# Kernel tuning notes

Measured on AMD Instinct MI355X. Metric: run time of the kernel, lower is better.

Reference implementation:

```python
import jax, jax.numpy as jnp
import numpy as np

N, F, H, D = 50000, 128, 8, 16   # nodes, node features, heads, per-head dim (F == H*D -> Identity residual)
E, G = 800000, 512               # edges, graphs
HD = H * D


def _xavier(key, shape):
    fan = sum(shape[-2:]) if len(shape) >= 2 else shape[0] + 1
    lim = (6.0 / (shape[-2] + shape[-1])) ** 0.5 if len(shape) >= 2 else (6.0 / fan) ** 0.5
    return jax.random.uniform(key, shape, jnp.float32, -lim, lim)


def setup_inputs() -> dict:
    key = jax.random.key(0)
    ks = jax.random.split(key, 10)
    x = jax.random.normal(ks[0], (N, F), jnp.float32)
    edge_index = jax.random.randint(ks[1], (2, E), 0, N, dtype=jnp.int64)
    batch = jnp.sort(jax.random.randint(ks[2], (N,), 0, G, dtype=jnp.int64))
    W_src = _xavier(ks[3], (HD, F))
    W_dst = _xavier(ks[4], (HD, F))
    double_attn = _xavier(ks[5], (1, H, D))  # xavier over last two dims
    bias = jnp.zeros((HD,), jnp.float32)
    prelu_alpha = jnp.float32(0.25)          # nn.PReLU() default single weight
    w_weighting = _xavier(ks[6], (1, HD))
    b_weighting = jnp.zeros((1,), jnp.float32)
    w_score = _xavier(ks[7], (HD, HD))
    b_score = jnp.zeros((HD,), jnp.float32)
    return {
        "x": x, "edge_index": edge_index, "batch": batch,
        "W_src": W_src, "W_dst": W_dst, "double_attn": double_attn,
        "bias": bias, "prelu_alpha": prelu_alpha,
        "w_weighting": w_weighting, "b_weighting": b_weighting,
        "w_score": w_score, "b_score": b_score,
    }


def reference(x, edge_index, batch, W_src, W_dst, double_attn, bias, prelu_alpha,
              w_weighting, b_weighting, w_score, b_score):
    src, dst = edge_index[0], edge_index[1]
    # dropout is identity in eval mode
    src_p = (x @ W_src.T).reshape(N, H, D)    # [N,H,D]
    dst_p = (x @ W_dst.T).reshape(N, H, D)
    # edge-wise attention logits: gather + LeakyReLU(0.2) + dot with attention vector
    e = src_p[src] + dst_p[dst]               # [E,H,D]
    e = jnp.where(e > 0, e, 0.2 * e)
    logits = jnp.einsum('ehd,ohd->eh', e, double_attn)  # [E,H] (double_attn has leading 1)
    # segment softmax over destination nodes (global max shift, as in original)
    exp = jnp.exp(logits - logits.max())
    denom = jax.ops.segment_sum(exp, dst, num_segments=N)  # [N,H]
    alpha = exp / (denom[dst] + 1e-16)        # [E,H]
    # weighted aggregation of source projections
    msg = src_p[src] * alpha[:, :, None]      # [E,H,D]
    out = jax.ops.segment_sum(msg, dst, num_segments=N)    # [N,H,D]
    out = out + x.reshape(N, H, D)            # residual (Identity since F == H*D)
    out = out.reshape(N, HD) + bias           # concat heads + bias
    out = jnp.where(out > 0, out, prelu_alpha * out)       # PReLU activation
    # ReadoutPhase: gated sum pooling + max pooling per graph, concatenated
    weighted = jax.nn.sigmoid(out @ w_weighting.T + b_weighting)  # [N,1]
    score = out @ w_score.T + b_score                              # [N,HD]
    g_sum = jax.ops.segment_sum(weighted * score, batch, num_segments=G)  # [G,HD]
    g_max = jax.ops.segment_max(out, batch, num_segments=G)              # [G,HD]
    readout = jnp.concatenate([g_sum, g_max], axis=1)                     # [G,2*HD]
    return out, readout
```

## Files before the change

kernel.cpp:

```cpp
#include <hip/hip_runtime.h>

#define NODES 50000
#define FEAT 128
#define EDGES 800000
#define GRAPHS 512
#define NB 196
#define CHUNK 4096
#define ABLK 196
#define BCAP 8192
#define PROJ_BLOCKS 782

typedef unsigned int u32;
typedef unsigned short u16;
typedef __attribute__((ext_vector_type(8))) short short8;
typedef __attribute__((ext_vector_type(4))) float v4f;
typedef __attribute__((ext_vector_type(4))) u32 u32x4;
typedef __attribute__((ext_vector_type(2))) float f2;

static __device__ __forceinline__ float bflo(u32 u){ return __uint_as_float(u << 16); }
static __device__ __forceinline__ float bfhi(u32 u){ return __uint_as_float(u & 0xffff0000u); }
static __device__ __forceinline__ u16 f2bf(float f){
  u32 u = __float_as_uint(f);
  u32 r = u + 0x7fffu + ((u >> 16) & 1u);
  return (u16)(r >> 16);
}
static __device__ __forceinline__ u32 packbf(float a, float b){
  return (u32)f2bf(a) | ((u32)f2bf(b) << 16);
}
static __device__ __forceinline__ f2 unpk(u32 u){ f2 r; r.x = bflo(u); r.y = bfhi(u); return r; }
static __device__ __forceinline__ f2 vmax2(f2 a, f2 b){ f2 r; r.x = fmaxf(a.x,b.x); r.y = fmaxf(a.y,b.y); return r; }

#define LROW 68
__global__ __launch_bounds__(256) void proj_hist_kernel(
    const float* __restrict__ x, const float* __restrict__ Wsrc,
    const float* __restrict__ Wdst, u16* __restrict__ srcp, u16* __restrict__ dstp,
    const int* __restrict__ ei, int* __restrict__ bcount)
{
  __shared__ u32 x_lds[64 * LROW];
  __shared__ int cnt[NB];
  const int t = threadIdx.x;

  if (blockIdx.x >= PROJ_BLOCKS){
    const int b = blockIdx.x - PROJ_BLOCKS;
    for (int k = t; k < NB; k += 256) cnt[k] = 0;
    __syncthreads();
    const int e0 = b * CHUNK;
    const int e1 = (e0 + CHUNK < EDGES) ? e0 + CHUNK : EDGES;
    for (int e = e0 + t; e < e1; e += 256)
      atomicAdd(&cnt[ei[EDGES + e] >> 8], 1);
    __syncthreads();
    for (int k = t; k < NB; k += 256) bcount[k * ABLK + b] = cnt[k];
    return;
  }

  const int node0 = blockIdx.x * 64;
  const int rows_valid = NODES - node0 < 64 ? NODES - node0 : 64;
  const float4* xp = (const float4*)(x + (size_t)node0 * 128);
  for (int idx = t; idx < rows_valid * 32; idx += 256){
    const float4 v = xp[idx];
    const int row = idx >> 5, cq = idx & 31;
    x_lds[row * LROW + cq * 2]     = packbf(v.x, v.y);
    x_lds[row * LROW + cq * 2 + 1] = packbf(v.z, v.w);
  }

  const int wave = t >> 6, lane = t & 63;
  const int r16 = lane & 15;
  const int quad = lane >> 4;
  const int ko = quad * 4;
  const int n0 = wave * 32;

  short8 bs[2][4], bd[2][4];
  #pragma unroll
  for (int nt = 0; nt < 2; ++nt){
    const int col = n0 + nt * 16 + r16;
    #pragma unroll
    for (int k = 0; k < 4; ++k){
      const float4* wp = (const float4*)(Wsrc + col * 128 + quad * 8 + k * 32);
      float4 w0 = wp[0], w1 = wp[1];
      u32x4 pk; pk.x = packbf(w0.x,w0.y); pk.y = packbf(w0.z,w0.w);
      pk.z = packbf(w1.x,w1.y); pk.w = packbf(w1.z,w1.w);
      bs[nt][k] = __builtin_bit_cast(short8, pk);
      const float4* vp = (const float4*)(Wdst + col * 128 + quad * 8 + k * 32);
      float4 v0 = vp[0], v1 = vp[1];
      u32x4 qk; qk.x = packbf(v0.x,v0.y); qk.y = packbf(v0.z,v0.w);
      qk.z = packbf(v1.x,v1.y); qk.w = packbf(v1.z,v1.w);
      bd[nt][k] = __builtin_bit_cast(short8, qk);
    }
  }
  __syncthreads();

  #pragma unroll
  for (int mt = 0; mt < 4; ++mt){
    const int node_base = node0 + mt * 16;
    if (node_base >= NODES) break;
    short8 afr[4];
    #pragma unroll
    for (int k = 0; k < 4; ++k)
      afr[k] = *(const short8*)&x_lds[(mt * 16 + r16) * LROW + ko + k * 16];
    v4f s0 = {0.f,0.f,0.f,0.f}, s1 = s0, d0 = s0, d1 = s0;
    #pragma unroll
    for (int k = 0; k < 4; ++k){
      s0 = __builtin_amdgcn_mfma_f32_16x16x32_bf16(afr[k], bs[0][k], s0, 0, 0, 0);
      s1 = __builtin_amdgcn_mfma_f32_16x16x32_bf16(afr[k], bs[1][k], s1, 0, 0, 0);
      d0 = __builtin_amdgcn_mfma_f32_16x16x32_bf16(afr[k], bd[0][k], d0, 0, 0, 0);
      d1 = __builtin_amdgcn_mfma_f32_16x16x32_bf16(afr[k], bd[1][k], d1, 0, 0, 0);
    }
    u16* so = srcp + (size_t)(node_base + quad * 4) * 128 + n0 + r16;
    u16* do_ = dstp + (size_t)(node_base + quad * 4) * 128 + n0 + r16;
    #pragma unroll
    for (int r = 0; r < 4; ++r){
      so[r * 128]      = f2bf(s0[r]);
      so[r * 128 + 16] = f2bf(s1[r]);
      do_[r * 128]      = f2bf(d0[r]);
      do_[r * 128 + 16] = f2bf(d1[r]);
    }
  }
}

__global__ __launch_bounds__(256) void bucket_scatter_kernel(
    const int* __restrict__ ei, const int* __restrict__ bcount,
    int* __restrict__ bstart_g, u32* __restrict__ ebuf)
{
  __shared__ int tot[256];
  __shared__ int bstart_s[NB + 1];
  __shared__ int obase_s[NB];
  __shared__ int cur[NB];
  const int b = blockIdx.x, t = threadIdx.x;
  int total = 0, obase = 0;
  if (t < NB){
    const int* row = bcount + t * ABLK;
    int run = 0;
    for (int q = 0; q < ABLK; ++q){
      if (q == b) obase = run;
      run += row[q];
    }
    total = run;
  }
  tot[t] = total;
  __syncthreads();
  const int v = total;
  for (int off = 1; off < 256; off <<= 1){
    const int add = (t >= off) ? tot[t - off] : 0;
    __syncthreads();
    tot[t] += add;
    __syncthreads();
  }
  if (t < NB){
    bstart_s[t] = tot[t] - v;
    obase_s[t] = obase;
    cur[t] = 0;
  }
  if (t == NB - 1) bstart_s[NB] = tot[t];
  __syncthreads();
  if (b == 0 && t <= NB) bstart_g[t] = bstart_s[t];

  const int e0 = b * CHUNK;
  const int e1 = (e0 + CHUNK < EDGES) ? e0 + CHUNK : EDGES;
  for (int e = e0 + t; e < e1; e += 256){
    const int d = ei[EDGES + e];
    const int s = ei[e];
    const int k = d >> 8;
    const int r = atomicAdd(&cur[k], 1);
    ebuf[bstart_s[k] + obase_s[k] + r] = (u32)s | ((u32)(d & 255) << 16);
  }
}

__global__ __launch_bounds__(256) void bucket_csr_kernel(
    const u32* __restrict__ ebuf, const int* __restrict__ bstart,
    int* __restrict__ row_start, int* __restrict__ srclist)
{
  __shared__ int cnt[256], excl[256], cur[256];
  __shared__ u32 loc[BCAP];
  const int k = blockIdx.x, t = threadIdx.x;
  const int base = bstart[k];
  int ne = bstart[k + 1] - base;
  if (ne > BCAP) ne = BCAP;
  cnt[t] = 0;
  __syncthreads();
  for (int j = t; j < ne; j += 256)
    atomicAdd(&cnt[(ebuf[base + j] >> 16) & 255], 1);
  __syncthreads();
  const int v = cnt[t];
  for (int off = 1; off < 256; off <<= 1){
    const int add = (t >= off) ? cnt[t - off] : 0;
    __syncthreads();
    cnt[t] += add;
    __syncthreads();
  }
  excl[t] = cnt[t] - v;
  cur[t] = cnt[t] - v;
  __syncthreads();
  const int node = k * 256 + t;
  if (node <= NODES) row_start[node] = base + excl[t];
  for (int j = t; j < ne; j += 256){
    const u32 e = ebuf[base + j];
    const int p = atomicAdd(&cur[(e >> 16) & 255], 1);
    loc[p] = e & 0xFFFFu;
  }
  __syncthreads();
  for (int j = t; j < ne; j += 256)
    srclist[base + j] = (int)loc[j];
}

__global__ __launch_bounds__(256, 4) void aggregate_kernel(
    const u16* __restrict__ srcp, const u16* __restrict__ dstp,
    const int* __restrict__ row_start, const int* __restrict__ srclist,
    const float* __restrict__ x, const float* __restrict__ attn,
    const float* __restrict__ bias, const float* __restrict__ palpha,
    const float* __restrict__ ww, const float* __restrict__ bw,
    float* __restrict__ outp, float* __restrict__ weighted)
{
  const int wv = threadIdx.x >> 6;
  const int lane = threadIdx.x & 63;
  const int half = lane >> 5;
  const int l32 = lane & 31;
  const int h = lane & 7;
  const int es = (lane >> 3) & 3;
  const int i = (blockIdx.x * 4 + wv) * 2 + half;
  const uint4* sp = (const uint4*)srcp;

  f2 d2[8], a2[8];
  {
    const uint4 dA = ((const uint4*)dstp)[(size_t)i * 16 + h * 2];
    const uint4 dB = ((const uint4*)dstp)[(size_t)i * 16 + h * 2 + 1];
    d2[0]=unpk(dA.x); d2[1]=unpk(dA.y); d2[2]=unpk(dA.z); d2[3]=unpk(dA.w);
    d2[4]=unpk(dB.x); d2[5]=unpk(dB.y); d2[6]=unpk(dB.z); d2[7]=unpk(dB.w);
    const float4* ap = (const float4*)attn + h * 4;
    #pragma unroll
    for (int q = 0; q < 4; ++q){
      const float4 vv = ap[q];
      a2[2*q].x = vv.x; a2[2*q].y = vv.y; a2[2*q+1].x = vv.z; a2[2*q+1].y = vv.w;
    }
  }
  const int lo = row_start[i], hi = row_start[i + 1];
  const int deg = hi - lo;
  int myidx = 0;
  if (l32 < deg) myidx = srclist[lo + l32];
  const int nb = (deg + 3) >> 2;

  f2 acc2[8];
  #pragma unroll
  for (int k = 0; k < 8; ++k){ acc2[k].x = 0.f; acc2[k].y = 0.f; }
  float denom = 0.f;

  auto FETCH = [&](int k, uint4& A, uint4& B, bool& v){
    const int il = k * 4 + es;
    v = il < deg;
    int s;
    if (il < 32) s = __shfl(myidx, half * 32 + il);
    else         s = v ? srclist[lo + il] : 0;
    if (!v) s = 0;
    const uint4* rp = sp + (size_t)s * 16 + h * 2;
    A = rp[0]; B = rp[1];
  };

  uint4 cA, cB, nA, nB, mA, mB;
  bool cv = false, nv = false, mv = false;
  if (nb > 0) FETCH(0, cA, cB, cv);
  if (nb > 1) FETCH(1, nA, nB, nv);
  for (int k = 0; k < nb; ++k){
    if (k + 2 < nb) FETCH(k + 2, mA, mB, mv); else mv = false;
    f2 sv[8];
    sv[0]=unpk(cA.x); sv[1]=unpk(cA.y); sv[2]=unpk(cA.z); sv[3]=unpk(cA.w);
    sv[4]=unpk(cB.x); sv[5]=unpk(cB.y); sv[6]=unpk(cB.z); sv[7]=unpk(cB.w);
    f2 p; p.x = 0.f; p.y = 0.f;
    #pragma unroll
    for (int q = 0; q < 8; ++q){
      f2 e = sv[q] + d2[q];
      e = vmax2(e, e * 0.2f);
      p += e * a2[q];
    }
    float w = cv ? __expf(p.x + p.y) : 0.f;
    denom += w;
    f2 w2; w2.x = w; w2.y = w;
    #pragma unroll
    for (int q = 0; q < 8; ++q) acc2[q] += sv[q] * w2;
    cA = nA; cB = nB; cv = nv;
    nA = mA; nB = mB; nv = mv;
  }
  #pragma unroll
  for (int m = 8; m <= 16; m <<= 1){
    #pragma unroll
    for (int q = 0; q < 8; ++q){
      acc2[q].x += __shfl_xor(acc2[q].x, m);
      acc2[q].y += __shfl_xor(acc2[q].y, m);
    }
    denom += __shfl_xor(denom, m);
  }
  const float inv = 1.f / (denom + 1e-16f);

  const float al = palpha[0];
  float o[16];
  {
    const float4* xp = (const float4*)x + (size_t)i * 32 + h * 4;
    const float4* bp = (const float4*)bias + h * 4;
    #pragma unroll
    for (int q = 0; q < 4; ++q){
      const float4 xv = xp[q];
      const float4 bv = bp[q];
      float t0 = fmaf(acc2[2*q].x,   inv, xv.x) + bv.x;
      float t1 = fmaf(acc2[2*q].y,   inv, xv.y) + bv.y;
      float t2 = fmaf(acc2[2*q+1].x, inv, xv.z) + bv.z;
      float t3 = fmaf(acc2[2*q+1].y, inv, xv.w) + bv.w;
      o[4*q]   = (t0 > 0.f) ? t0 : al * t0;
      o[4*q+1] = (t1 > 0.f) ? t1 : al * t1;
      o[4*q+2] = (t2 > 0.f) ? t2 : al * t2;
      o[4*q+3] = (t3 > 0.f) ? t3 : al * t3;
    }
  }
  if (es == 0){
    float4* op = (float4*)outp + (size_t)i * 32 + h * 4;
    #pragma unroll
    for (int q = 0; q < 4; ++q){
      float4 vv; vv.x = o[4*q]; vv.y = o[4*q+1]; vv.z = o[4*q+2]; vv.w = o[4*q+3];
      op[q] = vv;
    }
  }
  float z = 0.f;
  {
    const float4* gp = (const float4*)ww + h * 4;
    #pragma unroll
    for (int q = 0; q < 4; ++q){
      const float4 gv = gp[q];
      z = fmaf(o[4*q], gv.x, z); z = fmaf(o[4*q+1], gv.y, z);
      z = fmaf(o[4*q+2], gv.z, z); z = fmaf(o[4*q+3], gv.w, z);
    }
  }
  z += __shfl_xor(z, 1);
  z += __shfl_xor(z, 2);
  z += __shfl_xor(z, 4);
  if (l32 == 0){
    z += bw[0];
    weighted[i] = 1.f / (1.f + __expf(-z));
  }
}

__global__ __launch_bounds__(256) void readout_kernel(
    const float* __restrict__ outp, const float* __restrict__ weighted,
    const int* __restrict__ batchv, const float* __restrict__ wscore,
    const float* __restrict__ bscore, float* __restrict__ ro)
{
  __shared__ int range_s[2];
  __shared__ float wsum_s[128];
  __shared__ float max_s[128];
  __shared__ float wtot_s[2];
  __shared__ float part_s[256];
  const int g = blockIdx.x, t = threadIdx.x;
  const int col = t & 127, grp = t >> 7;
  if (t < 2){
    const int target = g + t;
    int lo = 0, hi = NODES;
    while (lo < hi){ const int m = (lo + hi) >> 1; if (batchv[m] < target) lo = m + 1; else hi = m; }
    range_s[t] = lo;
  }
  __syncthreads();
  const int lo = range_s[0], hi = range_s[1];
  float acc = 0.f, vmax = -INFINITY, wacc = 0.f;
  for (int n = lo + grp; n < hi; n += 2){
    const float w = weighted[n];
    const float v = outp[n * 128 + col];
    acc = fmaf(w, v, acc);
    vmax = fmaxf(vmax, v);
    if (col == 0) wacc += w;
  }
  part_s[t] = acc;
  if (col == 0) wtot_s[grp] = wacc;
  __syncthreads();
  if (grp == 0) wsum_s[col] = acc + part_s[col + 128];
  __syncthreads();
  part_s[t] = vmax;
  __syncthreads();
  if (grp == 0) max_s[col] = fmaxf(vmax, part_s[col + 128]);
  const float wtot = wtot_s[0] + wtot_s[1];
  __syncthreads();
  float dot = 0.f;
  const float* wr = wscore + col * 128 + grp * 64;
  const float* xs = wsum_s + grp * 64;
  #pragma unroll
  for (int k = 0; k < 64; ++k) dot = fmaf(wr[k], xs[k], dot);
  part_s[t] = dot;
  __syncthreads();
  if (grp == 0){
    const float s = dot + part_s[col + 128] + wtot * bscore[col];
    ro[g * 256 + col] = s;
    ro[g * 256 + 128 + col] = max_s[col];
  }
}

extern "C" void kernel_launch(void* const* d_in, const int* in_sizes, int n_in,
                              void* d_out, int out_size, void* d_ws, size_t ws_size,
                              hipStream_t stream)
{
  const float* x      = (const float*)d_in[0];
  const int*   ei     = (const int*)d_in[1];
  const int*   batchv = (const int*)d_in[2];
  const float* Wsrc   = (const float*)d_in[3];
  const float* Wdst   = (const float*)d_in[4];
  const float* attn   = (const float*)d_in[5];
  const float* bias   = (const float*)d_in[6];
  const float* palpha = (const float*)d_in[7];
  const float* ww     = (const float*)d_in[8];
  const float* bw     = (const float*)d_in[9];
  const float* wsc    = (const float*)d_in[10];
  const float* bsc    = (const float*)d_in[11];

  char* ws = (char*)d_ws;
  u16*  srcp      = (u16*) (ws + 0);
  u16*  dstp      = (u16*) (ws + 12800000);
  int*  srclist   = (int*) (ws + 25600000);
  int*  row_start = (int*) (ws + 28800000);
  int*  bcount    = (int*) (ws + 29000192);
  int*  bstart    = (int*) (ws + 29153856);
  float* weighted = (float*)(ws + 29154688);

  float* outp = (float*)d_out;
  float* ro = outp + NODES * FEAT;
  u32* ebuf = (u32*)d_out;

  proj_hist_kernel<<<PROJ_BLOCKS + ABLK, 256, 0, stream>>>(
      x, Wsrc, Wdst, srcp, dstp, ei, bcount);
  bucket_scatter_kernel<<<ABLK, 256, 0, stream>>>(ei, bcount, bstart, ebuf);
  bucket_csr_kernel<<<NB, 256, 0, stream>>>(ebuf, bstart, row_start, srclist);
  aggregate_kernel<<<6250, 256, 0, stream>>>(srcp, dstp, row_start, srclist,
                                             x, attn, bias, palpha, ww, bw,
                                             outp, weighted);
  readout_kernel<<<GRAPHS, 256, 0, stream>>>(outp, weighted, batchv, wsc, bsc, ro);
}
```

Before: 219.0 us.

## Unroll edge gather loop with four-deep prefetch and transpose bucket count layout

The per-node aggregation loop, previously a rolling two-ahead prefetch, becomes a fully unrolled schedule for up to 32 edges. Four row loads are in flight at once and the loop bound is made uniform across the two half-waves. Higher-degree nodes fall back to a simple serial loop. The bucket histogram is also stored block-major, so the scatter kernel's prefix scan reads it coalesced across threads. The aim is more memory-level parallelism in the gather, at the cost of extra registers and a slow tail for nodes with more than 32 in-edges.

```diff
diff --git a/kernel.cpp b/kernel.cpp
--- a/kernel.cpp
+++ b/kernel.cpp
@@ -49,7 +49,7 @@
     for (int e = e0 + t; e < e1; e += 256)
       atomicAdd(&cnt[ei[EDGES + e] >> 8], 1);
     __syncthreads();
-    for (int k = t; k < NB; k += 256) bcount[k * ABLK + b] = cnt[k];
+    for (int k = t; k < NB; k += 256) bcount[b * NB + k] = cnt[k];
     return;
   }
 
@@ -128,11 +128,10 @@
   const int b = blockIdx.x, t = threadIdx.x;
   int total = 0, obase = 0;
   if (t < NB){
-    const int* row = bcount + t * ABLK;
     int run = 0;
     for (int q = 0; q < ABLK; ++q){
       if (q == b) obase = run;
-      run += row[q];
+      run += bcount[q * NB + t];
     }
     total = run;
   }
@@ -237,32 +236,22 @@
   int myidx = 0;
   if (l32 < deg) myidx = srclist[lo + l32];
   const int nb = (deg + 3) >> 2;
+  int nbw = nb;
+  { const int ot = __shfl_xor(nb, 32); nbw = nbw > ot ? nbw : ot; }
 
   f2 acc2[8];
   #pragma unroll
-  for (int k = 0; k < 8; ++k){ acc2[k].x = 0.f; acc2[k].y = 0.f; }
+  for (int q = 0; q < 8; ++q){ acc2[q].x = 0.f; acc2[q].y = 0.f; }
   float denom = 0.f;
 
-  auto FETCH = [&](int k, uint4& A, uint4& B, bool& v){
-    const int il = k * 4 + es;
-    v = il < deg;
-    int s;
-    if (il < 32) s = __shfl(myidx, half * 32 + il);
-    else         s = v ? srclist[lo + il] : 0;
-    if (!v) s = 0;
+  auto LOADK = [&](int s, uint4& A, uint4& B){
     const uint4* rp = sp + (size_t)s * 16 + h * 2;
     A = rp[0]; B = rp[1];
   };
-
-  uint4 cA, cB, nA, nB, mA, mB;
-  bool cv = false, nv = false, mv = false;
-  if (nb > 0) FETCH(0, cA, cB, cv);
-  if (nb > 1) FETCH(1, nA, nB, nv);
-  for (int k = 0; k < nb; ++k){
-    if (k + 2 < nb) FETCH(k + 2, mA, mB, mv); else mv = false;
+  auto COMPV = [&](bool valid, const uint4& A, const uint4& B){
     f2 sv[8];
-    sv[0]=unpk(cA.x); sv[1]=unpk(cA.y); sv[2]=unpk(cA.z); sv[3]=unpk(cA.w);
-    sv[4]=unpk(cB.x); sv[5]=unpk(cB.y); sv[6]=unpk(cB.z); sv[7]=unpk(cB.w);
+    sv[0]=unpk(A.x); sv[1]=unpk(A.y); sv[2]=unpk(A.z); sv[3]=unpk(A.w);
+    sv[4]=unpk(B.x); sv[5]=unpk(B.y); sv[6]=unpk(B.z); sv[7]=unpk(B.w);
     f2 p; p.x = 0.f; p.y = 0.f;
     #pragma unroll
     for (int q = 0; q < 8; ++q){
@@ -270,14 +259,49 @@
       e = vmax2(e, e * 0.2f);
       p += e * a2[q];
     }
-    float w = cv ? __expf(p.x + p.y) : 0.f;
+    const float w = valid ? __expf(p.x + p.y) : 0.f;
     denom += w;
     f2 w2; w2.x = w; w2.y = w;
     #pragma unroll
     for (int q = 0; q < 8; ++q) acc2[q] += sv[q] * w2;
-    cA = nA; cB = nB; cv = nv;
-    nA = mA; nB = mB; nv = mv;
-  }
+  };
+
+  int s0,s1,s2,s3,s4,s5,s6,s7;
+  {
+    int t0;
+    t0 = __shfl(myidx, half*32 +  0 + es); s0 = ( 0 + es < deg) ? t0 : 0;
+    t0 = __shfl(myidx, half*32 +  4 + es); s1 = ( 4 + es < deg) ? t0 : 0;
+    t0 = __shfl(myidx, half*32 +  8 + es); s2 = ( 8 + es < deg) ? t0 : 0;
+    t0 = __shfl(myidx, half*32 + 12 + es); s3 = (12 + es < deg) ? t0 : 0;
+    t0 = __shfl(myidx, half*32 + 16 + es); s4 = (16 + es < deg) ? t0 : 0;
+    t0 = __shfl(myidx, half*32 + 20 + es); s5 = (20 + es < deg) ? t0 : 0;
+    t0 = __shfl(myidx, half*32 + 24 + es); s6 = (24 + es < deg) ? t0 : 0;
+    t0 = __shfl(myidx, half*32 + 28 + es); s7 = (28 + es < deg) ? t0 : 0;
+  }
+
+  uint4 A0,B0,A1,B1,A2,B2,A3,B3;
+  if (nbw > 0) LOADK(s0, A0, B0);
+  if (nbw > 1) LOADK(s1, A1, B1);
+  if (nbw > 2) LOADK(s2, A2, B2);
+  if (nbw > 3) LOADK(s3, A3, B3);
+  if (nbw > 0){ COMPV( 0 + es < deg, A0, B0); if (nbw > 4) LOADK(s4, A0, B0); }
+  if (nbw > 1){ COMPV( 4 + es < deg, A1, B1); if (nbw > 5) LOADK(s5, A1, B1); }
+  if (nbw > 2){ COMPV( 8 + es < deg, A2, B2); if (nbw > 6) LOADK(s6, A2, B2); }
+  if (nbw > 3){ COMPV(12 + es < deg, A3, B3); if (nbw > 7) LOADK(s7, A3, B3); }
+  if (nbw > 4) COMPV(16 + es < deg, A0, B0);
+  if (nbw > 5) COMPV(20 + es < deg, A1, B1);
+  if (nbw > 6) COMPV(24 + es < deg, A2, B2);
+  if (nbw > 7) COMPV(28 + es < deg, A3, B3);
+  if (nbw > 8){
+    for (int kk = 8; kk < nbw; ++kk){
+      const int il = kk * 4 + es;
+      const int s = (il < deg) ? srclist[lo + il] : 0;
+      uint4 TA, TB;
+      LOADK(s, TA, TB);
+      COMPV(il < deg, TA, TB);
+    }
+  }
+
   #pragma unroll
   for (int m = 8; m <= 16; m <<= 1){
     #pragma unroll
```

Measured after the change: 214.2 us. 1.02x faster.

## Store projections head-major and split aggregation per head across blocks

Applied to the files above, without the earlier changes.

Projections are now written in a head-major layout ([H][N][16] bf16), so each aggregate block handles one head and gathers only 32-byte rows, which is meant to improve cache locality per head. The aggregate kernel is launched with 8x more blocks, one head per block, and each 16-lane group splits a head's dimensions across lane pairs. The gating dot product is accumulated across heads with atomics into a zeroed buffer, and the sigmoid is moved into the readout kernel. Source lists shrink to u16, and the bcount layout is transposed. The source rows are gathered eight times over the whole launch, which adds block and atomic overhead. The u16 srclist relies on node ids fitting in 16 bits, and N=50000 does fit.

```diff
diff --git a/kernel.cpp b/kernel.cpp
--- a/kernel.cpp
+++ b/kernel.cpp
@@ -49,7 +49,7 @@
     for (int e = e0 + t; e < e1; e += 256)
       atomicAdd(&cnt[ei[EDGES + e] >> 8], 1);
     __syncthreads();
-    for (int k = t; k < NB; k += 256) bcount[k * ABLK + b] = cnt[k];
+    for (int k = t; k < NB; k += 256) bcount[b * NB + k] = cnt[k];
     return;
   }
 
@@ -105,34 +105,38 @@
       d0 = __builtin_amdgcn_mfma_f32_16x16x32_bf16(afr[k], bd[0][k], d0, 0, 0, 0);
       d1 = __builtin_amdgcn_mfma_f32_16x16x32_bf16(afr[k], bd[1][k], d1, 0, 0, 0);
     }
-    u16* so = srcp + (size_t)(node_base + quad * 4) * 128 + n0 + r16;
-    u16* do_ = dstp + (size_t)(node_base + quad * 4) * 128 + n0 + r16;
+    const int node = node_base + quad * 4;
+    u16* so0 = srcp + ((size_t)(wave*2)   * NODES + node) * 16 + r16;
+    u16* so1 = srcp + ((size_t)(wave*2+1) * NODES + node) * 16 + r16;
+    u16* dd0 = dstp + ((size_t)(wave*2)   * NODES + node) * 16 + r16;
+    u16* dd1 = dstp + ((size_t)(wave*2+1) * NODES + node) * 16 + r16;
     #pragma unroll
     for (int r = 0; r < 4; ++r){
-      so[r * 128]      = f2bf(s0[r]);
-      so[r * 128 + 16] = f2bf(s1[r]);
-      do_[r * 128]      = f2bf(d0[r]);
-      do_[r * 128 + 16] = f2bf(d1[r]);
+      so0[r * 16] = f2bf(s0[r]);
+      so1[r * 16] = f2bf(s1[r]);
+      dd0[r * 16] = f2bf(d0[r]);
+      dd1[r * 16] = f2bf(d1[r]);
     }
   }
 }
 
 __global__ __launch_bounds__(256) void bucket_scatter_kernel(
     const int* __restrict__ ei, const int* __restrict__ bcount,
-    int* __restrict__ bstart_g, u32* __restrict__ ebuf)
+    int* __restrict__ bstart_g, u32* __restrict__ ebuf, float* __restrict__ wsum)
 {
   __shared__ int tot[256];
   __shared__ int bstart_s[NB + 1];
   __shared__ int obase_s[NB];
   __shared__ int cur[NB];
   const int b = blockIdx.x, t = threadIdx.x;
+  const int nid = b * 256 + t;
+  if (nid < NODES) wsum[nid] = 0.f;
   int total = 0, obase = 0;
   if (t < NB){
-    const int* row = bcount + t * ABLK;
     int run = 0;
     for (int q = 0; q < ABLK; ++q){
       if (q == b) obase = run;
-      run += row[q];
+      run += bcount[q * NB + t];
     }
     total = run;
   }
@@ -167,7 +171,7 @@
 
 __global__ __launch_bounds__(256) void bucket_csr_kernel(
     const u32* __restrict__ ebuf, const int* __restrict__ bstart,
-    int* __restrict__ row_start, int* __restrict__ srclist)
+    int* __restrict__ row_start, u16* __restrict__ srclist)
 {
   __shared__ int cnt[256], excl[256], cur[256];
   __shared__ u32 loc[BCAP];
@@ -199,146 +203,137 @@
   }
   __syncthreads();
   for (int j = t; j < ne; j += 256)
-    srclist[base + j] = (int)loc[j];
-}
-
-__global__ __launch_bounds__(256, 4) void aggregate_kernel(
+    srclist[base + j] = (u16)loc[j];
+}
+
+__global__ __launch_bounds__(256) void aggregate_kernel(
     const u16* __restrict__ srcp, const u16* __restrict__ dstp,
-    const int* __restrict__ row_start, const int* __restrict__ srclist,
+    const int* __restrict__ row_start, const u16* __restrict__ srclist,
     const float* __restrict__ x, const float* __restrict__ attn,
     const float* __restrict__ bias, const float* __restrict__ palpha,
-    const float* __restrict__ ww, const float* __restrict__ bw,
-    float* __restrict__ outp, float* __restrict__ weighted)
-{
+    const float* __restrict__ ww, float* __restrict__ outp,
+    float* __restrict__ wsum)
+{
+  const int h   = blockIdx.x & 7;
+  const int grp = blockIdx.x >> 3;
   const int wv = threadIdx.x >> 6;
   const int lane = threadIdx.x & 63;
   const int half = lane >> 5;
   const int l32 = lane & 31;
-  const int h = lane & 7;
-  const int es = (lane >> 3) & 3;
-  const int i = (blockIdx.x * 4 + wv) * 2 + half;
+  const int es = l32 >> 1;
+  const int dh = lane & 1;
+  const int i = grp * 8 + wv * 2 + half;
+  const size_t hN = (size_t)h * NODES;
   const uint4* sp = (const uint4*)srcp;
 
-  f2 d2[8], a2[8];
+  f2 d2[4], a2[4];
   {
-    const uint4 dA = ((const uint4*)dstp)[(size_t)i * 16 + h * 2];
-    const uint4 dB = ((const uint4*)dstp)[(size_t)i * 16 + h * 2 + 1];
-    d2[0]=unpk(dA.x); d2[1]=unpk(dA.y); d2[2]=unpk(dA.z); d2[3]=unpk(dA.w);
-    d2[4]=unpk(dB.x); d2[5]=unpk(dB.y); d2[6]=unpk(dB.z); d2[7]=unpk(dB.w);
-    const float4* ap = (const float4*)attn + h * 4;
-    #pragma unroll
-    for (int q = 0; q < 4; ++q){
-      const float4 vv = ap[q];
-      a2[2*q].x = vv.x; a2[2*q].y = vv.y; a2[2*q+1].x = vv.z; a2[2*q+1].y = vv.w;
-    }
+    const uint4 dv = ((const uint4*)dstp)[(hN + i) * 2 + dh];
+    d2[0]=unpk(dv.x); d2[1]=unpk(dv.y); d2[2]=unpk(dv.z); d2[3]=unpk(dv.w);
+    const float4* ap = (const float4*)(attn + h * 16 + dh * 8);
+    const float4 a0 = ap[0], a1 = ap[1];
+    a2[0].x=a0.x; a2[0].y=a0.y; a2[1].x=a0.z; a2[1].y=a0.w;
+    a2[2].x=a1.x; a2[2].y=a1.y; a2[3].x=a1.z; a2[3].y=a1.w;
   }
   const int lo = row_start[i], hi = row_start[i + 1];
   const int deg = hi - lo;
   int myidx = 0;
-  if (l32 < deg) myidx = srclist[lo + l32];
-  const int nb = (deg + 3) >> 2;
-
-  f2 acc2[8];
-  #pragma unroll
-  for (int k = 0; k < 8; ++k){ acc2[k].x = 0.f; acc2[k].y = 0.f; }
+  if (l32 < deg) myidx = (int)srclist[lo + l32];
+  const int nb = (deg + 15) >> 4;
+  int nbw = nb; { const int o = __shfl_xor(nb, 32); if (o > nbw) nbw = o; }
+
+  f2 acc[4];
+  #pragma unroll
+  for (int q = 0; q < 4; ++q){ acc[q].x = 0.f; acc[q].y = 0.f; }
   float denom = 0.f;
 
-  auto FETCH = [&](int k, uint4& A, uint4& B, bool& v){
-    const int il = k * 4 + es;
-    v = il < deg;
-    int s;
-    if (il < 32) s = __shfl(myidx, half * 32 + il);
-    else         s = v ? srclist[lo + il] : 0;
-    if (!v) s = 0;
-    const uint4* rp = sp + (size_t)s * 16 + h * 2;
-    A = rp[0]; B = rp[1];
-  };
-
-  uint4 cA, cB, nA, nB, mA, mB;
-  bool cv = false, nv = false, mv = false;
-  if (nb > 0) FETCH(0, cA, cB, cv);
-  if (nb > 1) FETCH(1, nA, nB, nv);
-  for (int k = 0; k < nb; ++k){
-    if (k + 2 < nb) FETCH(k + 2, mA, mB, mv); else mv = false;
-    f2 sv[8];
-    sv[0]=unpk(cA.x); sv[1]=unpk(cA.y); sv[2]=unpk(cA.z); sv[3]=unpk(cA.w);
-    sv[4]=unpk(cB.x); sv[5]=unpk(cB.y); sv[6]=unpk(cB.z); sv[7]=unpk(cB.w);
+  auto COMP = [&](bool valid, const uint4& A){
+    f2 sv[4];
+    sv[0]=unpk(A.x); sv[1]=unpk(A.y); sv[2]=unpk(A.z); sv[3]=unpk(A.w);
     f2 p; p.x = 0.f; p.y = 0.f;
     #pragma unroll
-    for (int q = 0; q < 8; ++q){
+    for (int q = 0; q < 4; ++q){
       f2 e = sv[q] + d2[q];
       e = vmax2(e, e * 0.2f);
       p += e * a2[q];
     }
-    float w = cv ? __expf(p.x + p.y) : 0.f;
+    const float p8 = p.x + p.y;
+    const float lg = p8 + __shfl_xor(p8, 1);
+    const float w = valid ? __expf(lg) : 0.f;
     denom += w;
     f2 w2; w2.x = w; w2.y = w;
     #pragma unroll
-    for (int q = 0; q < 8; ++q) acc2[q] += sv[q] * w2;
-    cA = nA; cB = nB; cv = nv;
-    nA = mA; nB = mB; nv = mv;
-  }
-  #pragma unroll
-  for (int m = 8; m <= 16; m <<= 1){
-    #pragma unroll
-    for (int q = 0; q < 8; ++q){
-      acc2[q].x += __shfl_xor(acc2[q].x, m);
-      acc2[q].y += __shfl_xor(acc2[q].y, m);
-    }
-    denom += __shfl_xor(denom, m);
-  }
+    for (int q = 0; q < 4; ++q) acc[q] += sv[q] * w2;
+  };
+
+  int s0, s1; bool v0, v1;
+  { const int j = es;      v0 = j < deg; const int t0 = __shfl(myidx, half*32 + j); s0 = v0 ? t0 : 0; }
+  { const int j = 16 + es; v1 = j < deg; const int t1 = __shfl(myidx, half*32 + j); s1 = v1 ? t1 : 0; }
+
+  uint4 A0, A1;
+  if (nbw > 0) A0 = sp[(hN + s0) * 2 + dh];
+  if (nbw > 1) A1 = sp[(hN + s1) * 2 + dh];
+  if (nbw > 0) COMP(v0, A0);
+  if (nbw > 1) COMP(v1, A1);
+  if (nbw > 2){
+    for (int c = 2; c < nbw; ++c){
+      const int j = c * 16 + es;
+      const bool v = j < deg;
+      const int s = v ? (int)srclist[lo + j] : 0;
+      const uint4 A = sp[(hN + s) * 2 + dh];
+      COMP(v, A);
+    }
+  }
+
+  #pragma unroll
+  for (int m = 2; m <= 16; m <<= 1) denom += __shfl_xor(denom, m);
+
+  float af[8];
+  af[0]=acc[0].x; af[1]=acc[0].y; af[2]=acc[1].x; af[3]=acc[1].y;
+  af[4]=acc[2].x; af[5]=acc[2].y; af[6]=acc[3].x; af[7]=acc[3].y;
+  float b4[4];
+  #pragma unroll
+  for (int k = 0; k < 4; ++k){
+    const float give = (lane & 2) ? af[k] : af[4 + k];
+    const float got = __shfl_xor(give, 2);
+    b4[k] = ((lane & 2) ? af[4 + k] : af[k]) + got;
+  }
+  float c2[2];
+  #pragma unroll
+  for (int k = 0; k < 2; ++k){
+    const float give = (lane & 4) ? b4[k] : b4[2 + k];
+    const float got = __shfl_xor(give, 4);
+    c2[k] = ((lane & 4) ? b4[2 + k] : b4[k]) + got;
+  }
+  float d1;
+  {
+    const float give = (lane & 8) ? c2[0] : c2[1];
+    const float got = __shfl_xor(give, 8);
+    d1 = ((lane & 8) ? c2[1] : c2[0]) + got;
+  }
+  d1 += __shfl_xor(d1, 16);
+
   const float inv = 1.f / (denom + 1e-16f);
-
+  const int dim = dh * 8 + ((lane & 2) ? 4 : 0) + ((lane & 4) ? 2 : 0) + ((lane & 8) ? 1 : 0);
+  const int col = h * 16 + dim;
+  const float xr = x[(size_t)i * 128 + col];
+  const float bv = bias[col];
   const float al = palpha[0];
-  float o[16];
-  {
-    const float4* xp = (const float4*)x + (size_t)i * 32 + h * 4;
-    const float4* bp = (const float4*)bias + h * 4;
-    #pragma unroll
-    for (int q = 0; q < 4; ++q){
-      const float4 xv = xp[q];
-      const float4 bv = bp[q];
-      float t0 = fmaf(acc2[2*q].x,   inv, xv.x) + bv.x;
-      float t1 = fmaf(acc2[2*q].y,   inv, xv.y) + bv.y;
-      float t2 = fmaf(acc2[2*q+1].x, inv, xv.z) + bv.z;
-      float t3 = fmaf(acc2[2*q+1].y, inv, xv.w) + bv.w;
-      o[4*q]   = (t0 > 0.f) ? t0 : al * t0;
-      o[4*q+1] = (t1 > 0.f) ? t1 : al * t1;
-      o[4*q+2] = (t2 > 0.f) ? t2 : al * t2;
-      o[4*q+3] = (t3 > 0.f) ? t3 : al * t3;
-    }
-  }
-  if (es == 0){
-    float4* op = (float4*)outp + (size_t)i * 32 + h * 4;
-    #pragma unroll
-    for (int q = 0; q < 4; ++q){
-      float4 vv; vv.x = o[4*q]; vv.y = o[4*q+1]; vv.z = o[4*q+2]; vv.w = o[4*q+3];
-      op[q] = vv;
-    }
-  }
-  float z = 0.f;
-  {
-    const float4* gp = (const float4*)ww + h * 4;
-    #pragma unroll
-    for (int q = 0; q < 4; ++q){
-      const float4 gv = gp[q];
-      z = fmaf(o[4*q], gv.x, z); z = fmaf(o[4*q+1], gv.y, z);
-      z = fmaf(o[4*q+2], gv.z, z); z = fmaf(o[4*q+3], gv.w, z);
-    }
-  }
-  z += __shfl_xor(z, 1);
-  z += __shfl_xor(z, 2);
-  z += __shfl_xor(z, 4);
-  if (l32 == 0){
-    z += bw[0];
-    weighted[i] = 1.f / (1.f + __expf(-z));
-  }
+  float tv = fmaf(d1, inv, xr) + bv;
+  const float o = (tv > 0.f) ? tv : al * tv;
+  if ((lane & 16) == 0) outp[(size_t)i * 128 + col] = o;
+
+  float z = (lane & 16) ? 0.f : o * ww[col];
+  z += __shfl_xor(z, 1); z += __shfl_xor(z, 2); z += __shfl_xor(z, 4);
+  z += __shfl_xor(z, 8); z += __shfl_xor(z, 16);
+  if (l32 == 0) atomicAdd(&wsum[i], z);
 }
 
 __global__ __launch_bounds__(256) void readout_kernel(
-    const float* __restrict__ outp, const float* __restrict__ weighted,
-    const int* __restrict__ batchv, const float* __restrict__ wscore,
-    const float* __restrict__ bscore, float* __restrict__ ro)
+    const float* __restrict__ outp, const float* __restrict__ wsumv,
+    const int* __restrict__ batchv, const float* __restrict__ bw,
+    const float* __restrict__ wscore, const float* __restrict__ bscore,
+    float* __restrict__ ro)
 {
   __shared__ int range_s[2];
   __shared__ float wsum_s[128];
@@ -347,6 +342,7 @@
   __shared__ float part_s[256];
   const int g = blockIdx.x, t = threadIdx.x;
   const int col = t & 127, grp = t >> 7;
+  const float bw0 = bw[0];
   if (t < 2){
     const int target = g + t;
     int lo = 0, hi = NODES;
@@ -357,7 +353,7 @@
   const int lo = range_s[0], hi = range_s[1];
   float acc = 0.f, vmax = -INFINITY, wacc = 0.f;
   for (int n = lo + grp; n < hi; n += 2){
-    const float w = weighted[n];
+    const float w = 1.f / (1.f + __expf(-(wsumv[n] + bw0)));
     const float v = outp[n * 128 + col];
     acc = fmaf(w, v, acc);
     vmax = fmaxf(vmax, v);
@@ -407,11 +403,11 @@
   char* ws = (char*)d_ws;
   u16*  srcp      = (u16*) (ws + 0);
   u16*  dstp      = (u16*) (ws + 12800000);
-  int*  srclist   = (int*) (ws + 25600000);
+  u16*  srclist   = (u16*) (ws + 25600000);
   int*  row_start = (int*) (ws + 28800000);
   int*  bcount    = (int*) (ws + 29000192);
   int*  bstart    = (int*) (ws + 29153856);
-  float* weighted = (float*)(ws + 29154688);
+  float* wsum     = (float*)(ws + 29154688);
 
   float* outp = (float*)d_out;
   float* ro = outp + NODES * FEAT;
@@ -419,10 +415,10 @@
 
   proj_hist_kernel<<<PROJ_BLOCKS + ABLK, 256, 0, stream>>>(
       x, Wsrc, Wdst, srcp, dstp, ei, bcount);
-  bucket_scatter_kernel<<<ABLK, 256, 0, stream>>>(ei, bcount, bstart, ebuf);
+  bucket_scatter_kernel<<<ABLK, 256, 0, stream>>>(ei, bcount, bstart, ebuf, wsum);
   bucket_csr_kernel<<<NB, 256, 0, stream>>>(ebuf, bstart, row_start, srclist);
-  aggregate_kernel<<<6250, 256, 0, stream>>>(srcp, dstp, row_start, srclist,
-                                             x, attn, bias, palpha, ww, bw,
-                                             outp, weighted);
-  readout_kernel<<<GRAPHS, 256, 0, stream>>>(outp, weighted, batchv, wsc, bsc, ro);
-}
+  aggregate_kernel<<<(NODES / 8) * 8, 256, 0, stream>>>(srcp, dstp, row_start, srclist,
+                                                        x, attn, bias, palpha, ww,
+                                                        outp, wsum);
+  readout_kernel<<<GRAPHS, 256, 0, stream>>>(outp, wsum, batchv, bw, wsc, bsc, ro);
+}
```

Measured after the change: 255.6 us. 16.8% more time.
